# Kernel optimization log

Measured on AMD Instinct MI355X. Metric: run time of the kernel, lower is better.

The kernel has to match this reference:

```python
import jax, jax.numpy as jnp
import numpy as np

B, T, D, H, HS = 4, 2048, 512, 8, 64

def setup_inputs() -> dict:
    key = jax.random.key(0)
    ks = jax.random.split(key, 5)
    scale = 1.0 / np.sqrt(D)
    return {
        "x": jax.random.normal(ks[0], (B, T, D), dtype=jnp.float32),
        "Wq": jax.random.normal(ks[1], (H, D, HS), dtype=jnp.float32) * scale,
        "Wk": jax.random.normal(ks[2], (H, D, HS), dtype=jnp.float32) * scale,
        "Wv": jax.random.normal(ks[3], (H, D, HS), dtype=jnp.float32) * scale,
        "Wo": jax.random.normal(ks[4], (D, D), dtype=jnp.float32) * scale,
        "bo": jnp.zeros((D,), dtype=jnp.float32),
    }

def reference(x, Wq, Wk, Wv, Wo, bo):
    # Per-head projections (stacked heads) -> [B,H,T,HS]
    q = jnp.einsum('btd,hde->bhte', x, Wq)
    k = jnp.einsum('btd,hde->bhte', x, Wk)
    v = jnp.einsum('btd,hde->bhte', x, Wv)
    # Full TxT attention scores, scaled by head_size**-0.5
    scores = jnp.einsum('bhte,bhse->bhts', q, k) * (HS ** -0.5)
    att = jax.nn.softmax(scores, axis=-1)
    out = jnp.einsum('bhts,bhse->bhte', att, v)
    # Concat heads: [B,H,T,HS] -> [B,T,H*HS] == [B,T,D]
    out = jnp.transpose(out, (0, 2, 1, 3)).reshape(out.shape[0], out.shape[2], -1)
    # Output projection (nn.Linear with bias)
    return out @ Wo + bo
```

## Files before the change

### kernel.cpp

```cpp
#include <hip/hip_runtime.h>
#include <stdint.h>

#define B_   4
#define T_   2048
#define D_   512
#define H_   8
#define HS_  64

typedef __attribute__((ext_vector_type(8))) short bf16x8;
typedef __attribute__((ext_vector_type(4))) float f32x4;

__device__ __forceinline__ unsigned short f2bf(float f) {
  union { float f; unsigned u; } v; v.f = f;
  unsigned r = v.u + 0x7fffu + ((v.u >> 16) & 1u);
  return (unsigned short)(r >> 16);
}

__device__ __forceinline__ void gload_lds16(const void* g, void* l) {
  __builtin_amdgcn_global_load_lds(
      (const __attribute__((address_space(1))) void*)g,
      (__attribute__((address_space(3))) void*)l,
      16, 0, 0);
}

__global__ __launch_bounds__(256) void k_prep(
    const float* __restrict__ x,
    const float* __restrict__ Wq, const float* __restrict__ Wk,
    const float* __restrict__ Wv, const float* __restrict__ Wo,
    unsigned short* __restrict__ xb, unsigned short* __restrict__ Wtq,
    unsigned short* __restrict__ Wto)
{
  const int bid = blockIdx.x, tid = threadIdx.x;
  if (bid < 4096) {
    const int i = bid * 256 + tid;
    float4 v = ((const float4*)x)[i];
    ushort4 o;
    o.x = f2bf(v.x); o.y = f2bf(v.y); o.z = f2bf(v.z); o.w = f2bf(v.w);
    ((ushort4*)xb)[i] = o;
  } else if (bid < 7168) {
    const int idx = (bid - 4096) * 256 + tid;
    const int n = idx >> 9, d = idx & 511;
    const int proj = n >> 9, c = n & 511, h = c >> 6, e = c & 63;
    const float* W = (proj == 0) ? Wq : ((proj == 1) ? Wk : Wv);
    Wtq[idx] = f2bf(W[((h << 9) + d) * 64 + e]);
  } else {
    const int idx = (bid - 7168) * 256 + tid;
    const int n = idx >> 9, d = idx & 511;
    Wto[idx] = f2bf(Wo[(d << 9) + n]);
  }
}

template<int MODE>
__global__ __launch_bounds__(256) void k_gemm(
    const unsigned short* __restrict__ A, const unsigned short* __restrict__ Bt,
    unsigned short* __restrict__ Qb, unsigned short* __restrict__ Kb,
    unsigned short* __restrict__ Vp,
    const float* __restrict__ bo, float* __restrict__ Cout)
{
  const int m0 = blockIdx.y * 128, n0 = blockIdx.x * 128;
  __shared__ unsigned short At[128 * 32];
  __shared__ unsigned short Bs[128 * 32];
  const int tid = threadIdx.x, lane = tid & 63, wid = tid >> 6;
  const int wm = wid >> 1, wn = wid & 1;
  const int r16 = lane & 15, g = lane >> 4;

  f32x4 acc[4][4];
  const f32x4 fz = {0.f, 0.f, 0.f, 0.f};
#pragma unroll
  for (int i = 0; i < 4; ++i)
#pragma unroll
    for (int j = 0; j < 4; ++j) acc[i][j] = fz;

  for (int k0 = 0; k0 < 512; k0 += 32) {
#pragma unroll
    for (int j = 0; j < 2; ++j) {
      const int idx = j * 256 + tid;
      const int rr = idx >> 2, cc = (idx & 3) << 3;
      gload_lds16(A + (size_t)(m0 + rr) * 512 + k0 + cc, &At[(j * 256 + wid * 64) * 8]);
      gload_lds16(Bt + (size_t)(n0 + rr) * 512 + k0 + cc, &Bs[(j * 256 + wid * 64) * 8]);
    }
    __syncthreads();
    bf16x8 am[4], bn[4];
#pragma unroll
    for (int mi = 0; mi < 4; ++mi)
      am[mi] = *(const bf16x8*)&At[(wm * 64 + mi * 16 + r16) * 32 + g * 8];
#pragma unroll
    for (int ni = 0; ni < 4; ++ni)
      bn[ni] = *(const bf16x8*)&Bs[(wn * 64 + ni * 16 + r16) * 32 + g * 8];
#pragma unroll
    for (int mi = 0; mi < 4; ++mi)
#pragma unroll
      for (int ni = 0; ni < 4; ++ni)
        acc[mi][ni] = __builtin_amdgcn_mfma_f32_16x16x32_bf16(am[mi], bn[ni], acc[mi][ni], 0, 0, 0);
    __syncthreads();
  }

  const float QSC = 0.18033688f;
#pragma unroll
  for (int mi = 0; mi < 4; ++mi) {
#pragma unroll
    for (int ni = 0; ni < 4; ++ni) {
#pragma unroll
      for (int r = 0; r < 4; ++r) {
        const int m = m0 + wm * 64 + mi * 16 + g * 4 + r;
        const int n = n0 + wn * 64 + ni * 16 + r16;
        const float val = acc[mi][ni][r];
        if (MODE == 0) {
          const int proj = n >> 9, c = n & 511, h = c >> 6, e = c & 63;
          const int b = m >> 11, t = m & 2047;
          if (proj == 0) {
            Qb[(((size_t)(b * 8 + h) * 2048 + t) << 6) + e] = f2bf(val * QSC);
          } else if (proj == 1) {
            Kb[(((size_t)(b * 8 + h) * 2048 + t) << 6) + e] = f2bf(val);
          } else {
            const int kk = t & 31, tblk = t >> 5;
            const int j = (((kk >> 2) & 3) << 3) + ((kk >> 4) << 2) + (kk & 3);
            Vp[(((size_t)(b * 8 + h) << 6) + e) * 2048 + (tblk << 5) + j] = f2bf(val);
          }
        } else {
          Cout[(size_t)m * 512 + n] = val + bo[n];
        }
      }
    }
  }
}

#define DRAINBAR() do { \
    asm volatile("s_waitcnt vmcnt(0)" ::: "memory"); \
    __builtin_amdgcn_s_barrier(); \
    asm volatile("" ::: "memory"); } while (0)

__global__ __launch_bounds__(256, 3) void k_attn(
    const unsigned short* __restrict__ Qb, const unsigned short* __restrict__ Kb,
    const unsigned short* __restrict__ Vp, unsigned short* __restrict__ Ob)
{
  const int lin = blockIdx.x;
  const int xcd = lin & 7, slot = lin >> 3;
  const int bh = xcd * 4 + (slot & 3);
  const int qblk = slot >> 2;
  const int b = bh >> 3, h = bh & 7;

  const int tid = threadIdx.x, lane = tid & 63, wid = tid >> 6;
  const int q0 = qblk * 128 + wid * 32;
  const int r16 = lane & 15, g = lane >> 4;
  const int swz = r16 & 7;
  const unsigned short* Qh = Qb + (size_t)bh * T_ * 64;
  const unsigned short* Kh = Kb + (size_t)bh * T_ * 64;
  const unsigned short* Vh = Vp + (size_t)bh * 64 * T_;

  __shared__ unsigned short Ks[2][4096];
  __shared__ unsigned short Vs[2][4096];

  const bf16x8 qa00 = *(const bf16x8*)&Qh[(size_t)(q0 + r16) * 64 + g * 8];
  const bf16x8 qa01 = *(const bf16x8*)&Qh[(size_t)(q0 + r16) * 64 + 32 + g * 8];
  const bf16x8 qa10 = *(const bf16x8*)&Qh[(size_t)(q0 + 16 + r16) * 64 + g * 8];
  const bf16x8 qa11 = *(const bf16x8*)&Qh[(size_t)(q0 + 16 + r16) * 64 + 32 + g * 8];

  const f32x4 fz = {0.f, 0.f, 0.f, 0.f};
  f32x4 accA[4], accB[4];
#pragma unroll
  for (int eb = 0; eb < 4; ++eb) { accA[eb] = fz; accB[eb] = fz; }
  f32x4 accLA = fz, accLB = fz;

  bf16x8 onesv;
#pragma unroll
  for (int i = 0; i < 8; ++i) onesv[i] = (short)0x3F80;

  const int sb = wid * 8 + (lane >> 3);
  const int ssc = (lane & 7) ^ (lane >> 3);
  const unsigned short* kg = Kh + (size_t)sb * 64 + ssc * 8;
  const unsigned short* vg = Vh + (size_t)sb * T_ + ssc * 8;

  auto stage = [&](const unsigned short* kgp, const unsigned short* vgp, int bf) {
    gload_lds16(kgp,                   &Ks[bf][wid * 512]);
    gload_lds16(kgp + 32 * 64,         &Ks[bf][2048 + wid * 512]);
    gload_lds16(vgp,                   &Vs[bf][wid * 512]);
    gload_lds16(vgp + (size_t)32 * T_, &Vs[bf][2048 + wid * 512]);
  };

  auto compute = [&](int bf) {
#pragma unroll
    for (int sub = 0; sub < 2; ++sub) {
      const int rb = (sub * 32 + r16) * 64;
      const int c0 = (g ^ swz) << 3;
      const bf16x8 kf00 = *(const bf16x8*)&Ks[bf][rb + c0];
      const bf16x8 kf01 = *(const bf16x8*)&Ks[bf][rb + (c0 ^ 32)];
      const bf16x8 kf10 = *(const bf16x8*)&Ks[bf][rb + 1024 + c0];
      const bf16x8 kf11 = *(const bf16x8*)&Ks[bf][rb + 1024 + (c0 ^ 32)];
      f32x4 s0a = __builtin_amdgcn_mfma_f32_16x16x32_bf16(kf00, qa00, fz, 0, 0, 0);
      s0a = __builtin_amdgcn_mfma_f32_16x16x32_bf16(kf01, qa01, s0a, 0, 0, 0);
      f32x4 s1a = __builtin_amdgcn_mfma_f32_16x16x32_bf16(kf10, qa00, fz, 0, 0, 0);
      s1a = __builtin_amdgcn_mfma_f32_16x16x32_bf16(kf11, qa01, s1a, 0, 0, 0);
      f32x4 s0b = __builtin_amdgcn_mfma_f32_16x16x32_bf16(kf00, qa10, fz, 0, 0, 0);
      s0b = __builtin_amdgcn_mfma_f32_16x16x32_bf16(kf01, qa11, s0b, 0, 0, 0);
      f32x4 s1b = __builtin_amdgcn_mfma_f32_16x16x32_bf16(kf10, qa10, fz, 0, 0, 0);
      s1b = __builtin_amdgcn_mfma_f32_16x16x32_bf16(kf11, qa11, s1b, 0, 0, 0);

      float pa[8], pb[8];
#pragma unroll
      for (int r = 0; r < 4; ++r) {
        pa[r]     = exp2f(s0a[r]);
        pa[4 + r] = exp2f(s1a[r]);
        pb[r]     = exp2f(s0b[r]);
        pb[4 + r] = exp2f(s1b[r]);
      }
      union { bf16x8 v; unsigned u[4]; } puA, puB;
#pragma unroll
      for (int i = 0; i < 4; ++i) {
        asm("v_cvt_pk_bf16_f32 %0, %1, %2" : "=v"(puA.u[i]) : "v"(pa[2 * i]), "v"(pa[2 * i + 1]));
        asm("v_cvt_pk_bf16_f32 %0, %1, %2" : "=v"(puB.u[i]) : "v"(pb[2 * i]), "v"(pb[2 * i + 1]));
      }

#pragma unroll
      for (int eb = 0; eb < 4; ++eb) {
        const bf16x8 vf = *(const bf16x8*)&Vs[bf][(eb * 16 + r16) * 64 + (c0 ^ (sub << 5))];
        accA[eb] = __builtin_amdgcn_mfma_f32_16x16x32_bf16(vf, puA.v, accA[eb], 0, 0, 0);
        accB[eb] = __builtin_amdgcn_mfma_f32_16x16x32_bf16(vf, puB.v, accB[eb], 0, 0, 0);
      }
      accLA = __builtin_amdgcn_mfma_f32_16x16x32_bf16(onesv, puA.v, accLA, 0, 0, 0);
      accLB = __builtin_amdgcn_mfma_f32_16x16x32_bf16(onesv, puB.v, accLB, 0, 0, 0);
    }
  };

  stage(kg, vg, 0); kg += 4096; vg += 64;
  DRAINBAR();

#pragma unroll 1
  for (int t = 0; t < 32; t += 2) {
    stage(kg, vg, 1); kg += 4096; vg += 64;
    compute(0);
    DRAINBAR();
    if (t < 30) { stage(kg, vg, 0); kg += 4096; vg += 64; }
    compute(1);
    DRAINBAR();
  }

  const float invLA = 1.0f / accLA[0];
  const float invLB = 1.0f / accLB[0];
  unsigned short* OrowA = Ob + ((size_t)(b * 2048 + q0 + r16) << 9) + h * 64 + g * 4;
  unsigned short* OrowB = Ob + ((size_t)(b * 2048 + q0 + 16 + r16) << 9) + h * 64 + g * 4;
#pragma unroll
  for (int eb = 0; eb < 4; ++eb) {
    uint2 ow;
    asm("v_cvt_pk_bf16_f32 %0, %1, %2" : "=v"(ow.x)
        : "v"(accA[eb][0] * invLA), "v"(accA[eb][1] * invLA));
    asm("v_cvt_pk_bf16_f32 %0, %1, %2" : "=v"(ow.y)
        : "v"(accA[eb][2] * invLA), "v"(accA[eb][3] * invLA));
    *(uint2*)(OrowA + eb * 16) = ow;
    asm("v_cvt_pk_bf16_f32 %0, %1, %2" : "=v"(ow.x)
        : "v"(accB[eb][0] * invLB), "v"(accB[eb][1] * invLB));
    asm("v_cvt_pk_bf16_f32 %0, %1, %2" : "=v"(ow.y)
        : "v"(accB[eb][2] * invLB), "v"(accB[eb][3] * invLB));
    *(uint2*)(OrowB + eb * 16) = ow;
  }
}

extern "C" void kernel_launch(void* const* d_in, const int* in_sizes, int n_in,
                              void* d_out, int out_size, void* d_ws, size_t ws_size,
                              hipStream_t stream) {
  const float* x  = (const float*)d_in[0];
  const float* Wq = (const float*)d_in[1];
  const float* Wk = (const float*)d_in[2];
  const float* Wv = (const float*)d_in[3];
  const float* Wo = (const float*)d_in[4];
  const float* bo = (const float*)d_in[5];
  float* out = (float*)d_out;
  char* ws = (char*)d_ws;

  unsigned short* xb  = (unsigned short*)(ws);
  unsigned short* Wtq = (unsigned short*)(ws + 8388608);
  unsigned short* Wto = (unsigned short*)(ws + 9961472);
  unsigned short* Qb  = (unsigned short*)(ws + 10485760);
  unsigned short* Kb  = (unsigned short*)(ws + 18874368);
  unsigned short* Vp  = (unsigned short*)(ws + 27262976);
  unsigned short* Ob  = (unsigned short*)(ws + 35651584);

  k_prep    <<<8192, 256, 0, stream>>>(x, Wq, Wk, Wv, Wo, xb, Wtq, Wto);
  k_gemm<0> <<<dim3(12, 64), 256, 0, stream>>>(xb, Wtq, Qb, Kb, Vp, nullptr, nullptr);
  k_attn    <<<512, 256, 0, stream>>>(Qb, Kb, Vp, Ob);
  k_gemm<1> <<<dim3(4, 64), 256, 0, stream>>>(Ob, Wto, nullptr, nullptr, nullptr, bo, out);
}
```

Before: 110.3 us.

## Triple-buffer K/V tiles with partial vmcnt waits and raise MFMA wave priority

```diff
diff --git a/kernel.cpp b/kernel.cpp
--- a/kernel.cpp
+++ b/kernel.cpp
@@ -125,11 +125,6 @@
   }
 }
 
-#define DRAINBAR() do { \
-    asm volatile("s_waitcnt vmcnt(0)" ::: "memory"); \
-    __builtin_amdgcn_s_barrier(); \
-    asm volatile("" ::: "memory"); } while (0)
-
 __global__ __launch_bounds__(256, 3) void k_attn(
     const unsigned short* __restrict__ Qb, const unsigned short* __restrict__ Kb,
     const unsigned short* __restrict__ Vp, unsigned short* __restrict__ Ob)
@@ -148,8 +143,8 @@
   const unsigned short* Kh = Kb + (size_t)bh * T_ * 64;
   const unsigned short* Vh = Vp + (size_t)bh * 64 * T_;
 
-  __shared__ unsigned short Ks[2][4096];
-  __shared__ unsigned short Vs[2][4096];
+  __shared__ unsigned short Ks[3][4096];
+  __shared__ unsigned short Vs[3][4096];
 
   const bf16x8 qa00 = *(const bf16x8*)&Qh[(size_t)(q0 + r16) * 64 + g * 8];
   const bf16x8 qa01 = *(const bf16x8*)&Qh[(size_t)(q0 + r16) * 64 + 32 + g * 8];
@@ -187,6 +182,7 @@
       const bf16x8 kf01 = *(const bf16x8*)&Ks[bf][rb + (c0 ^ 32)];
       const bf16x8 kf10 = *(const bf16x8*)&Ks[bf][rb + 1024 + c0];
       const bf16x8 kf11 = *(const bf16x8*)&Ks[bf][rb + 1024 + (c0 ^ 32)];
+      __builtin_amdgcn_s_setprio(1);
       f32x4 s0a = __builtin_amdgcn_mfma_f32_16x16x32_bf16(kf00, qa00, fz, 0, 0, 0);
       s0a = __builtin_amdgcn_mfma_f32_16x16x32_bf16(kf01, qa01, s0a, 0, 0, 0);
       f32x4 s1a = __builtin_amdgcn_mfma_f32_16x16x32_bf16(kf10, qa00, fz, 0, 0, 0);
@@ -195,6 +191,7 @@
       s0b = __builtin_amdgcn_mfma_f32_16x16x32_bf16(kf01, qa11, s0b, 0, 0, 0);
       f32x4 s1b = __builtin_amdgcn_mfma_f32_16x16x32_bf16(kf10, qa10, fz, 0, 0, 0);
       s1b = __builtin_amdgcn_mfma_f32_16x16x32_bf16(kf11, qa11, s1b, 0, 0, 0);
+      __builtin_amdgcn_s_setprio(0);
 
       float pa[8], pb[8];
 #pragma unroll
@@ -211,6 +208,7 @@
         asm("v_cvt_pk_bf16_f32 %0, %1, %2" : "=v"(puB.u[i]) : "v"(pb[2 * i]), "v"(pb[2 * i + 1]));
       }
 
+      __builtin_amdgcn_s_setprio(1);
 #pragma unroll
       for (int eb = 0; eb < 4; ++eb) {
         const bf16x8 vf = *(const bf16x8*)&Vs[bf][(eb * 16 + r16) * 64 + (c0 ^ (sub << 5))];
@@ -219,21 +217,40 @@
       }
       accLA = __builtin_amdgcn_mfma_f32_16x16x32_bf16(onesv, puA.v, accLA, 0, 0, 0);
       accLB = __builtin_amdgcn_mfma_f32_16x16x32_bf16(onesv, puB.v, accLB, 0, 0, 0);
+      __builtin_amdgcn_s_setprio(0);
     }
   };
 
+#define WAIT_N(lit) do { \
+    asm volatile("s_waitcnt vmcnt(" #lit ")" ::: "memory"); \
+    __builtin_amdgcn_sched_barrier(0); } while (0)
+
   stage(kg, vg, 0); kg += 4096; vg += 64;
-  DRAINBAR();
+  stage(kg, vg, 1); kg += 4096; vg += 64;
+  WAIT_N(0);
+  __builtin_amdgcn_s_barrier();
 
 #pragma unroll 1
-  for (int t = 0; t < 32; t += 2) {
-    stage(kg, vg, 1); kg += 4096; vg += 64;
-    compute(0);
-    DRAINBAR();
-    if (t < 30) { stage(kg, vg, 0); kg += 4096; vg += 64; }
-    compute(1);
-    DRAINBAR();
-  }
+  for (int k9 = 0; k9 < 10; ++k9) {
+#define PHASE(RB, SB) do { \
+    stage(kg, vg, SB); kg += 4096; vg += 64; \
+    WAIT_N(8); \
+    __builtin_amdgcn_s_barrier(); \
+    compute(RB); \
+    __builtin_amdgcn_s_barrier(); } while (0)
+    PHASE(0, 2);
+    PHASE(1, 0);
+    PHASE(2, 1);
+#undef PHASE
+  }
+  WAIT_N(4);
+  __builtin_amdgcn_s_barrier();
+  compute(0);
+  __builtin_amdgcn_s_barrier();
+  WAIT_N(0);
+  __builtin_amdgcn_s_barrier();
+  compute(1);
+#undef WAIT_N
 
   const float invLA = 1.0f / accLA[0];
   const float invLB = 1.0f / accLB[0];
```

Result: no change. 111.4 us (+0.9%).
